# Optimization experiments

Hardware: AMD Instinct MI355X
Metric: run time of the kernel (lower is better)

Reference implementation:

```python
import jax, jax.numpy as jnp
import numpy as np

OUT, IN = 8192, 8192
GROUP = 128
N_GROUPS = IN // GROUP
BATCH = 64


def dequant_int4(packed, scales):
    # packed: [OUT, IN//2] int32 bytes in [0,256); two 4-bit codes per byte
    low = packed & 0xF            # first element of each pair
    high = (packed >> 4) & 0xF    # second element
    q = jnp.stack([low, high], axis=-1).reshape(OUT, IN)  # interleaved nibbles
    # symmetric grouped dequant: w = (q - 8) * scale, scale per [row, group]
    qg = q.reshape(OUT, N_GROUPS, GROUP).astype(scales.dtype)
    w = (qg - 8.0) * scales[:, :, None]
    return w.reshape(OUT, IN)


def setup_inputs() -> dict:
    key = jax.random.key(0)
    k1, k2, k3 = jax.random.split(key, 3)
    x = jax.random.normal(k1, (BATCH, IN), dtype=jnp.float32)
    packed = jax.random.randint(k2, (OUT, IN // 2), 0, 256, dtype=jnp.int32)
    scales = jax.random.uniform(k3, (OUT, N_GROUPS), dtype=jnp.float32)
    return {"x": x, "packed": packed, "scales": scales}


def reference(x, packed, scales):
    # Dequantize int4 weights then dense matmul (F.linear, no bias)
    w = dequant_int4(packed, scales)        # [OUT, IN]
    return jnp.einsum('bi,oi->bo', x, w)    # [BATCH, OUT]
```

## Files before the change

kernel.cpp:

```cpp
#include <hip/hip_runtime.h>
#include <hip/hip_bf16.h>
#include <stdint.h>

#define OUTN   8192
#define INN    8192
#define NGRP   64
#define BATCHN 64
#define BN     128
#define BK     128
#define KSPLIT 8
#define KCHUNK (INN / KSPLIT)
#define NITER  (KCHUNK / BK)

typedef __attribute__((ext_vector_type(8))) short bf16x8;
typedef __attribute__((ext_vector_type(4))) float f32x4;
typedef __attribute__((ext_vector_type(4))) unsigned int u32x4;

__device__ __forceinline__ unsigned short f2bf(float f) {
  __hip_bfloat16 h = __float2bfloat16(f);
  return __builtin_bit_cast(unsigned short, h);
}
__device__ __forceinline__ float bf2f(unsigned short h) {
  unsigned int u = ((unsigned int)h) << 16;
  return __builtin_bit_cast(float, u);
}

__global__ void qlin_prep(const float* __restrict__ x, float* __restrict__ xsum) {
  const int b = blockIdx.x;
  const int t = threadIdx.x;
  const float* xrow = x + (size_t)b * INN + t * 32;
  float s = 0.0f;
#pragma unroll
  for (int i = 0; i < 8; ++i) {
    float4 v = *(const float4*)(xrow + i * 4);
    s += bf2f(f2bf(v.x)) + bf2f(f2bf(v.y)) + bf2f(f2bf(v.z)) + bf2f(f2bf(v.w));
  }
  __shared__ float part[256];
  part[t] = s;
  __syncthreads();
  if (t < NGRP) {
    float g = part[4 * t] + part[4 * t + 1] + part[4 * t + 2] + part[4 * t + 3];
    xsum[t * BATCHN + b] = g;
  }
}

__global__ __launch_bounds__(256, 2) void qlin_main(
    const float* __restrict__ x, const int* __restrict__ packed,
    const float* __restrict__ scales, const float* __restrict__ xsum,
    float* __restrict__ out) {
  const int bx    = blockIdx.x;
  const int ks    = bx & (KSPLIT - 1);
  const int ntile = bx >> 3;
  const int o0    = ntile * BN;
  const int g0    = ks * NITER;
  const int k0    = ks * KCHUNK;

  const int t    = threadIdx.x;
  const int lane = t & 63;
  const int w    = t >> 6;
  const int l15  = lane & 15;
  const int quad = lane >> 4;

  __shared__ __align__(16) int            pk[BN][68];
  __shared__ __align__(16) unsigned short xt[BATCHN][136];
  __shared__ __align__(16) float          st[BN][9];
  __shared__ __align__(16) float          xs[NITER][BATCHN];

#pragma unroll
  for (int i = 0; i < 4; ++i) {
    int v = t * 4 + i;
    int ol = v >> 3, gl = v & 7;
    st[ol][gl] = scales[(size_t)(o0 + ol) * NGRP + g0 + gl];
  }
#pragma unroll
  for (int i = 0; i < 2; ++i) {
    int v = t * 2 + i;
    int gl = v >> 6, b = v & 63;
    xs[gl][b] = xsum[(g0 + gl) * BATCHN + b];
  }

  int4   pkr[8];
  float4 xr[8];

  auto load_tile = [&](int i) {
    const int kk2 = ks * (KCHUNK / 2) + i * (BK / 2);
    const int* pbase = packed + (size_t)(o0 + (t >> 4)) * (INN / 2) + kk2 + (t & 15) * 4;
#pragma unroll
    for (int j = 0; j < 8; ++j)
      pkr[j] = *(const int4*)(pbase + (size_t)j * 16 * (INN / 2));
    const int kk = k0 + i * BK;
    const float* xbase = x + (size_t)(t >> 5) * INN + kk + (t & 31) * 4;
#pragma unroll
    for (int j = 0; j < 8; ++j)
      xr[j] = *(const float4*)(xbase + (size_t)j * 8 * INN);
  };

  auto store_tile = [&]() {
    const int prow = t >> 4, pcol = (t & 15) * 4;
#pragma unroll
    for (int j = 0; j < 8; ++j)
      *(int4*)&pk[prow + 16 * j][pcol] = pkr[j];
    const int xrow = t >> 5, xcol = (t & 31) * 4;
#pragma unroll
    for (int j = 0; j < 8; ++j) {
      ushort4 h;
      h.x = f2bf(xr[j].x); h.y = f2bf(xr[j].y);
      h.z = f2bf(xr[j].z); h.w = f2bf(xr[j].w);
      *(ushort4*)&xt[xrow + 8 * j][xcol] = h;
    }
  };

  f32x4 facc[4][2];
#pragma unroll
  for (int mt = 0; mt < 4; ++mt)
#pragma unroll
    for (int nt = 0; nt < 2; ++nt)
      facc[mt][nt] = (f32x4){0.f, 0.f, 0.f, 0.f};

  load_tile(0);

  for (int i = 0; i < NITER; ++i) {
    __syncthreads();
    store_tile();
    if (i + 1 < NITER) load_tile(i + 1);
    __syncthreads();

    f32x4 gacc[4][2];
#pragma unroll
    for (int mt = 0; mt < 4; ++mt)
#pragma unroll
      for (int nt = 0; nt < 2; ++nt)
        gacc[mt][nt] = (f32x4){0.f, 0.f, 0.f, 0.f};

#pragma unroll
    for (int kq = 0; kq < 4; ++kq) {
      bf16x8 af[4];
#pragma unroll
      for (int mt = 0; mt < 4; ++mt)
        af[mt] = *(const bf16x8*)&xt[mt * 16 + l15][kq * 32 + quad * 8];

      bf16x8 bfv[2];
#pragma unroll
      for (int nt = 0; nt < 2; ++nt) {
        int4 v4 = *(const int4*)&pk[w * 32 + nt * 16 + l15][kq * 16 + quad * 4];
        u32x4 bw;
        bw.x = 0x43004300u | ((unsigned)v4.x & 0xFu) | (((unsigned)v4.x & 0xF0u) << 12);
        bw.y = 0x43004300u | ((unsigned)v4.y & 0xFu) | (((unsigned)v4.y & 0xF0u) << 12);
        bw.z = 0x43004300u | ((unsigned)v4.z & 0xFu) | (((unsigned)v4.z & 0xF0u) << 12);
        bw.w = 0x43004300u | ((unsigned)v4.w & 0xFu) | (((unsigned)v4.w & 0xF0u) << 12);
        bfv[nt] = __builtin_bit_cast(bf16x8, bw);
      }
#pragma unroll
      for (int mt = 0; mt < 4; ++mt)
#pragma unroll
        for (int nt = 0; nt < 2; ++nt)
          gacc[mt][nt] = __builtin_amdgcn_mfma_f32_16x16x32_bf16(
              af[mt], bfv[nt], gacc[mt][nt], 0, 0, 0);
    }

    float s0 = st[w * 32 + l15][i];
    float s1 = st[w * 32 + 16 + l15][i];
#pragma unroll
    for (int mt = 0; mt < 4; ++mt) {
      f32x4 xv = *(const f32x4*)&xs[i][mt * 16 + quad * 4];
#pragma unroll
      for (int r = 0; r < 4; ++r) {
        float t0 = gacc[mt][0][r] - 136.0f * xv[r];
        float t1 = gacc[mt][1][r] - 136.0f * xv[r];
        facc[mt][0][r] += s0 * t0;
        facc[mt][1][r] += s1 * t1;
      }
    }
  }

  const int obase = o0 + w * 32 + l15;
#pragma unroll
  for (int mt = 0; mt < 4; ++mt)
#pragma unroll
    for (int r = 0; r < 4; ++r) {
      int m = mt * 16 + quad * 4 + r;
#pragma unroll
      for (int nt = 0; nt < 2; ++nt)
        atomicAdd(&out[(size_t)m * OUTN + obase + nt * 16], facc[mt][nt][r]);
    }
}

extern "C" void kernel_launch(void* const* d_in, const int* in_sizes, int n_in,
                              void* d_out, int out_size, void* d_ws, size_t ws_size,
                              hipStream_t stream) {
  const float* x      = (const float*)d_in[0];
  const int*   packed = (const int*)d_in[1];
  const float* scales = (const float*)d_in[2];
  float* out  = (float*)d_out;
  float* xsum = (float*)d_ws;

  hipMemsetAsync(d_out, 0, (size_t)out_size * sizeof(float), stream);
  qlin_prep<<<BATCHN, 256, 0, stream>>>(x, xsum);
  qlin_main<<<(OUTN / BN) * KSPLIT, 256, 0, stream>>>(x, packed, scales, xsum, out);
}
```

Before: 228.9 us.

## Halve output tile, compact packed nibbles in LDS, add split-K partial reduction

The output tile shrinks from 128 to 64 columns, doubling the grid and raising launch bounds to 4 blocks per CU for more parallelism. Packed int4 bytes are compacted into one 32-bit word per four bytes in LDS, which shrinks shared memory and the LDS reads per MFMA. When the workspace is large enough, each K-split writes partial results to a buffer and a separate reduce kernel sums them, replacing the atomics and the output memset. The cost is x being reloaded twice as often per weight column, and an extra 16 MB of partial-buffer traffic plus a kernel launch.

```diff
diff --git a/kernel.cpp b/kernel.cpp
--- a/kernel.cpp
+++ b/kernel.cpp
@@ -6,11 +6,12 @@
 #define INN    8192
 #define NGRP   64
 #define BATCHN 64
-#define BN     128
+#define BN     64
 #define BK     128
 #define KSPLIT 8
 #define KCHUNK (INN / KSPLIT)
 #define NITER  (KCHUNK / BK)
+#define OSZ    (BATCHN * OUTN)
 
 typedef __attribute__((ext_vector_type(8))) short bf16x8;
 typedef __attribute__((ext_vector_type(4))) float f32x4;
@@ -44,16 +45,18 @@
   }
 }
 
-__global__ __launch_bounds__(256, 2) void qlin_main(
+#define PKS 17
+#define XTS 136
+
+__global__ __launch_bounds__(256, 4) void qlin_main(
     const float* __restrict__ x, const int* __restrict__ packed,
     const float* __restrict__ scales, const float* __restrict__ xsum,
-    float* __restrict__ out) {
+    float* __restrict__ out, float* __restrict__ part) {
   const int bx    = blockIdx.x;
   const int ks    = bx & (KSPLIT - 1);
   const int ntile = bx >> 3;
   const int o0    = ntile * BN;
   const int g0    = ks * NITER;
-  const int k0    = ks * KCHUNK;
 
   const int t    = threadIdx.x;
   const int lane = t & 63;
@@ -61,61 +64,58 @@
   const int l15  = lane & 15;
   const int quad = lane >> 4;
 
-  __shared__ __align__(16) int            pk[BN][68];
-  __shared__ __align__(16) unsigned short xt[BATCHN][136];
+  __shared__ __align__(16) unsigned int   pk_c[BN * PKS];
+  __shared__ __align__(16) unsigned short xt[BATCHN * XTS];
   __shared__ __align__(16) float          st[BN][9];
   __shared__ __align__(16) float          xs[NITER][BATCHN];
 
 #pragma unroll
-  for (int i = 0; i < 4; ++i) {
-    int v = t * 4 + i;
+  for (int i = 0; i < 2; ++i) {
+    int v = t * 2 + i;
     int ol = v >> 3, gl = v & 7;
     st[ol][gl] = scales[(size_t)(o0 + ol) * NGRP + g0 + gl];
-  }
-#pragma unroll
-  for (int i = 0; i < 2; ++i) {
-    int v = t * 2 + i;
-    int gl = v >> 6, b = v & 63;
-    xs[gl][b] = xsum[(g0 + gl) * BATCHN + b];
-  }
-
-  int4   pkr[8];
+    int gl2 = v >> 6, b2 = v & 63;
+    xs[gl2][b2] = xsum[(g0 + gl2) * BATCHN + b2];
+  }
+
+  int4   pkr[4];
   float4 xr[8];
+
+  const int prow = t >> 4, pcol = t & 15;
+  const int xrow = t >> 5, xcol = t & 31;
 
   auto load_tile = [&](int i) {
     const int kk2 = ks * (KCHUNK / 2) + i * (BK / 2);
-    const int* pbase = packed + (size_t)(o0 + (t >> 4)) * (INN / 2) + kk2 + (t & 15) * 4;
+    const int* pbase = packed + (size_t)(o0 + prow) * (INN / 2) + kk2 + pcol * 4;
+#pragma unroll
+    for (int j = 0; j < 4; ++j)
+      pkr[j] = *(const int4*)(pbase + (size_t)(16 * j) * (INN / 2));
+    const int kk = ks * KCHUNK + i * BK;
+    const float* xbase = x + (size_t)xrow * INN + kk + xcol * 4;
 #pragma unroll
     for (int j = 0; j < 8; ++j)
-      pkr[j] = *(const int4*)(pbase + (size_t)j * 16 * (INN / 2));
-    const int kk = k0 + i * BK;
-    const float* xbase = x + (size_t)(t >> 5) * INN + kk + (t & 31) * 4;
-#pragma unroll
-    for (int j = 0; j < 8; ++j)
-      xr[j] = *(const float4*)(xbase + (size_t)j * 8 * INN);
+      xr[j] = *(const float4*)(xbase + (size_t)(8 * j) * INN);
   };
 
   auto store_tile = [&]() {
-    const int prow = t >> 4, pcol = (t & 15) * 4;
-#pragma unroll
-    for (int j = 0; j < 8; ++j)
-      *(int4*)&pk[prow + 16 * j][pcol] = pkr[j];
-    const int xrow = t >> 5, xcol = (t & 31) * 4;
+#pragma unroll
+    for (int j = 0; j < 4; ++j) {
+      unsigned int c = (unsigned)pkr[j].x | ((unsigned)pkr[j].y << 8) |
+                       ((unsigned)pkr[j].z << 16) | ((unsigned)pkr[j].w << 24);
+      pk_c[(prow + 16 * j) * PKS + pcol] = c;
+    }
 #pragma unroll
     for (int j = 0; j < 8; ++j) {
       ushort4 h;
       h.x = f2bf(xr[j].x); h.y = f2bf(xr[j].y);
       h.z = f2bf(xr[j].z); h.w = f2bf(xr[j].w);
-      *(ushort4*)&xt[xrow + 8 * j][xcol] = h;
+      *(ushort4*)&xt[(xrow + 8 * j) * XTS + xcol * 4] = h;
     }
   };
 
-  f32x4 facc[4][2];
-#pragma unroll
-  for (int mt = 0; mt < 4; ++mt)
-#pragma unroll
-    for (int nt = 0; nt < 2; ++nt)
-      facc[mt][nt] = (f32x4){0.f, 0.f, 0.f, 0.f};
+  f32x4 facc[4];
+#pragma unroll
+  for (int mt = 0; mt < 4; ++mt) facc[mt] = (f32x4){0.f, 0.f, 0.f, 0.f};
 
   load_tile(0);
 
@@ -125,64 +125,70 @@
     if (i + 1 < NITER) load_tile(i + 1);
     __syncthreads();
 
-    f32x4 gacc[4][2];
-#pragma unroll
-    for (int mt = 0; mt < 4; ++mt)
-#pragma unroll
-      for (int nt = 0; nt < 2; ++nt)
-        gacc[mt][nt] = (f32x4){0.f, 0.f, 0.f, 0.f};
+    f32x4 gacc[4];
+#pragma unroll
+    for (int mt = 0; mt < 4; ++mt) gacc[mt] = (f32x4){0.f, 0.f, 0.f, 0.f};
 
 #pragma unroll
     for (int kq = 0; kq < 4; ++kq) {
       bf16x8 af[4];
 #pragma unroll
       for (int mt = 0; mt < 4; ++mt)
-        af[mt] = *(const bf16x8*)&xt[mt * 16 + l15][kq * 32 + quad * 8];
-
-      bf16x8 bfv[2];
-#pragma unroll
-      for (int nt = 0; nt < 2; ++nt) {
-        int4 v4 = *(const int4*)&pk[w * 32 + nt * 16 + l15][kq * 16 + quad * 4];
-        u32x4 bw;
-        bw.x = 0x43004300u | ((unsigned)v4.x & 0xFu) | (((unsigned)v4.x & 0xF0u) << 12);
-        bw.y = 0x43004300u | ((unsigned)v4.y & 0xFu) | (((unsigned)v4.y & 0xF0u) << 12);
-        bw.z = 0x43004300u | ((unsigned)v4.z & 0xFu) | (((unsigned)v4.z & 0xF0u) << 12);
-        bw.w = 0x43004300u | ((unsigned)v4.w & 0xFu) | (((unsigned)v4.w & 0xF0u) << 12);
-        bfv[nt] = __builtin_bit_cast(bf16x8, bw);
-      }
+        af[mt] = *(const bf16x8*)&xt[(mt * 16 + l15) * XTS + kq * 32 + quad * 8];
+
+      unsigned int c = pk_c[(w * 16 + l15) * PKS + kq * 4 + quad];
+      u32x4 bw;
+      bw.x = 0x43004300u | (c & 0xFu) | ((c & 0xF0u) << 12);
+      bw.y = 0x43004300u | ((c >> 8) & 0xFu) | (((c >> 8) & 0xF0u) << 12);
+      bw.z = 0x43004300u | ((c >> 16) & 0xFu) | (((c >> 16) & 0xF0u) << 12);
+      bw.w = 0x43004300u | ((c >> 24) & 0xFu) | (((c >> 24) & 0xF0u) << 12);
+      bf16x8 bfv = __builtin_bit_cast(bf16x8, bw);
+
 #pragma unroll
       for (int mt = 0; mt < 4; ++mt)
-#pragma unroll
-        for (int nt = 0; nt < 2; ++nt)
-          gacc[mt][nt] = __builtin_amdgcn_mfma_f32_16x16x32_bf16(
-              af[mt], bfv[nt], gacc[mt][nt], 0, 0, 0);
-    }
-
-    float s0 = st[w * 32 + l15][i];
-    float s1 = st[w * 32 + 16 + l15][i];
+        gacc[mt] = __builtin_amdgcn_mfma_f32_16x16x32_bf16(af[mt], bfv, gacc[mt], 0, 0, 0);
+    }
+
+    float s0 = st[w * 16 + l15][i];
 #pragma unroll
     for (int mt = 0; mt < 4; ++mt) {
       f32x4 xv = *(const f32x4*)&xs[i][mt * 16 + quad * 4];
 #pragma unroll
+      for (int r = 0; r < 4; ++r)
+        facc[mt][r] += s0 * (gacc[mt][r] - 136.0f * xv[r]);
+    }
+  }
+
+  const int obase = o0 + w * 16 + l15;
+  if (part) {
+    float* pb = part + (size_t)ks * OSZ;
+#pragma unroll
+    for (int mt = 0; mt < 4; ++mt)
+#pragma unroll
       for (int r = 0; r < 4; ++r) {
-        float t0 = gacc[mt][0][r] - 136.0f * xv[r];
-        float t1 = gacc[mt][1][r] - 136.0f * xv[r];
-        facc[mt][0][r] += s0 * t0;
-        facc[mt][1][r] += s1 * t1;
+        int m = mt * 16 + quad * 4 + r;
+        pb[(size_t)m * OUTN + obase] = facc[mt][r];
       }
-    }
-  }
-
-  const int obase = o0 + w * 32 + l15;
-#pragma unroll
-  for (int mt = 0; mt < 4; ++mt)
-#pragma unroll
-    for (int r = 0; r < 4; ++r) {
-      int m = mt * 16 + quad * 4 + r;
-#pragma unroll
-      for (int nt = 0; nt < 2; ++nt)
-        atomicAdd(&out[(size_t)m * OUTN + obase + nt * 16], facc[mt][nt][r]);
-    }
+  } else {
+#pragma unroll
+    for (int mt = 0; mt < 4; ++mt)
+#pragma unroll
+      for (int r = 0; r < 4; ++r) {
+        int m = mt * 16 + quad * 4 + r;
+        atomicAdd(&out[(size_t)m * OUTN + obase], facc[mt][r]);
+      }
+  }
+}
+
+__global__ void qlin_reduce(const float* __restrict__ part, float* __restrict__ out) {
+  const size_t i = ((size_t)blockIdx.x * 256 + threadIdx.x) * 4;
+  float4 s = *(const float4*)(part + i);
+#pragma unroll
+  for (int ks = 1; ks < KSPLIT; ++ks) {
+    float4 v = *(const float4*)(part + (size_t)ks * OSZ + i);
+    s.x += v.x; s.y += v.y; s.z += v.z; s.w += v.w;
+  }
+  *(float4*)(out + i) = s;
 }
 
 extern "C" void kernel_launch(void* const* d_in, const int* in_sizes, int n_in,
@@ -193,8 +199,14 @@
   const float* scales = (const float*)d_in[2];
   float* out  = (float*)d_out;
   float* xsum = (float*)d_ws;
-
-  hipMemsetAsync(d_out, 0, (size_t)out_size * sizeof(float), stream);
+  const size_t part_off = 16384 / sizeof(float);
+  const size_t need = 16384 + (size_t)KSPLIT * OSZ * sizeof(float);
+  float* part = (ws_size >= need) ? ((float*)d_ws + part_off) : nullptr;
+
   qlin_prep<<<BATCHN, 256, 0, stream>>>(x, xsum);
-  qlin_main<<<(OUTN / BN) * KSPLIT, 256, 0, stream>>>(x, packed, scales, xsum, out);
-}
+  if (!part)
+    hipMemsetAsync(d_out, 0, (size_t)out_size * sizeof(float), stream);
+  qlin_main<<<(OUTN / BN) * KSPLIT, 256, 0, stream>>>(x, packed, scales, xsum, out, part);
+  if (part)
+    qlin_reduce<<<OSZ / 4 / 256, 256, 0, stream>>>(part, out);
+}
```

After: 207.9 us. -9.2%, faster.
